# Kernel optimization log

Measured on AMD Instinct MI355X. Metric: run time of the kernel, lower is better.

The kernel has to match this reference:

```python
import jax, jax.numpy as jnp
import numpy as np


def _maxpool3d(x):
    # 3x3x3 max pool, stride 1, padding 1 (torch pads with -inf for max pool)
    return jax.lax.reduce_window(
        x, -jnp.inf, jax.lax.max,
        window_dimensions=(1, 1, 3, 3, 3),
        window_strides=(1, 1, 1, 1, 1),
        padding=[(0, 0), (0, 0), (1, 1), (1, 1), (1, 1)],
    )


def _soft_erode(x):
    return -_maxpool3d(-x)


def _soft_dilate(x):
    return _maxpool3d(x)


def _soft_open(x):
    return _soft_dilate(_soft_erode(x))


def setup_inputs() -> dict:
    key = jax.random.key(0)
    img = jax.random.uniform(key, (2, 1, 192, 256, 256), dtype=jnp.float32)
    return {"img": img}


def reference(img):
    # NOTE: in the original torch module, `skel` is computed via soft_close +
    # an iterative relu(skel - soft_open(skel)) loop, but the final line
    # `skel = F.relu(img - soft_open(img))` overwrites it entirely, so the
    # loop is dead code and the output depends only on img.
    opened = _soft_open(img)  # dilate(erode(img)), morphological opening
    return jax.nn.relu(img - opened)
```

## Files before the change

### kernel.cpp

```cpp
#include <hip/hip_runtime.h>
#include <math.h>


#define D_ 192
#define H_ 256
#define W_ 256
#define NB 2
#define TH 32
#define TW 64
#define CD 16
#define NCHUNK (D_ / CD)

#define RAW_H (TH + 4)
#define RAW_W (TW + 8)
#define RAW_S 76
#define EB_H  (TH + 2)
#define EB_W  (TW + 8)
#define EB_S  76

#define NRAWF4 (RAW_H * (RAW_W / 4))
#define NBTASK (EB_H * (EB_W / 8))

__device__ __forceinline__ float min3f(float a, float b, float c) {
    return fminf(fminf(a, b), c);
}
__device__ __forceinline__ float max3f(float a, float b, float c) {
    return fmaxf(fmaxf(a, b), c);
}

__global__ __launch_bounds__(256, 3)
void soft_skel_v2(const float* __restrict__ img, float* __restrict__ out) {
    __shared__ __align__(16) float raw[RAW_H][RAW_S];
    __shared__ __align__(16) float ebuf[EB_H][EB_S];

    const int tid = threadIdx.x;
    const int w0 = blockIdx.x * TW;
    const int h0 = blockIdx.y * TH;
    const int n  = blockIdx.z / NCHUNK;
    const int ch = blockIdx.z - n * NCHUNK;
    const int z0 = ch * CD;

    const float* vol  = img + (size_t)n * (D_ * H_ * W_);
    float*       ovol = out + (size_t)n * (D_ * H_ * W_);

    const float PINF = INFINITY;

    bool a_slot[3], a_img[3];
    int  a_lds[3], a_off[3];
    #pragma unroll
    for (int k = 0; k < 3; ++k) {
        int idx = tid + 256 * k;
        bool slot = idx < NRAWF4;
        int row = idx / (RAW_W / 4);
        int cg  = idx - row * (RAW_W / 4);
        int gh = h0 - 2 + row;
        int gw = w0 - 4 + 4 * cg;
        a_slot[k] = slot;
        a_img[k]  = slot && (gh >= 0) && (gh < H_) && (gw >= 0) && (gw <= W_ - 4);
        a_off[k]  = gh * W_ + gw;
        a_lds[k]  = slot ? (row * RAW_S + 4 * cg) : 0;
    }

    const int  r0 = tid / 9;
    const int  c0 = (tid - r0 * 9) * 8;
    const bool has1 = tid < (NBTASK - 256);
    const int  t1 = tid + 256;
    const int  r1 = t1 / 9;
    const int  c1 = (t1 - r1 * 9) * 8;

    const int ty = tid >> 3;
    const int xx = (tid & 7) * 8;

    float pm0[8], sp0[8], pm1[8], sp1[8];
    float t2A[8], t2B[8], t2C[8];
    float rwA[8], rwB[8], rwC[8];
    #pragma unroll
    for (int j = 0; j < 8; ++j) {
        pm0[j] = sp0[j] = pm1[j] = sp1[j] = PINF;
        t2A[j] = t2B[j] = 0.f;
        rwA[j] = rwB[j] = 0.f;
    }

    auto prefetch = [&](int zz, float4 L[3]) {
        const bool zok = (zz >= 0) && (zz < D_);
        const float* plane = vol + (size_t)zz * (H_ * W_);
        #pragma unroll
        for (int k = 0; k < 3; ++k) {
            float4 v = make_float4(PINF, PINF, PINF, PINF);
            if (zok && a_img[k]) v = *(const float4*)(plane + a_off[k]);
            L[k] = v;
        }
    };

    auto btask = [&](int r, int cb, float pm[8], float sp[8], bool zeok) {
        float vm[10];
        {
            const float* p0 = &raw[r][0];
            const float* p1 = &raw[r + 1][0];
            const float* p2 = &raw[r + 2][0];
            int cl = cb - 1; if (cl < 0) cl = 0;
            int cr = cb + 8; if (cr > RAW_W - 1) cr = RAW_W - 1;
            vm[0] = min3f(p0[cl], p1[cl], p2[cl]);
            vm[9] = min3f(p0[cr], p1[cr], p2[cr]);
            float4 q00 = *(const float4*)(p0 + cb);
            float4 q01 = *(const float4*)(p0 + cb + 4);
            float4 q10 = *(const float4*)(p1 + cb);
            float4 q11 = *(const float4*)(p1 + cb + 4);
            float4 q20 = *(const float4*)(p2 + cb);
            float4 q21 = *(const float4*)(p2 + cb + 4);
            vm[1] = min3f(q00.x, q10.x, q20.x);
            vm[2] = min3f(q00.y, q10.y, q20.y);
            vm[3] = min3f(q00.z, q10.z, q20.z);
            vm[4] = min3f(q00.w, q10.w, q20.w);
            vm[5] = min3f(q01.x, q11.x, q21.x);
            vm[6] = min3f(q01.y, q11.y, q21.y);
            vm[7] = min3f(q01.z, q11.z, q21.z);
            vm[8] = min3f(q01.w, q11.w, q21.w);
        }
        float s[8];
        #pragma unroll
        for (int j = 0; j < 8; ++j) s[j] = min3f(vm[j], vm[j + 1], vm[j + 2]);

        const bool rok = zeok && ((unsigned)(h0 - 1 + r) < (unsigned)H_);
        float e[8];
        #pragma unroll
        for (int j = 0; j < 8; ++j) {
            float ev = fminf(pm[j], s[j]);
            bool ok = rok && ((unsigned)(w0 - 4 + cb + j) < (unsigned)W_);
            e[j] = ok ? ev : -PINF;
            pm[j] = fminf(sp[j], s[j]);
            sp[j] = s[j];
        }
        *(float4*)&ebuf[r][cb]     = make_float4(e[0], e[1], e[2], e[3]);
        *(float4*)&ebuf[r][cb + 4] = make_float4(e[4], e[5], e[6], e[7]);
    };

    float4 L[3];
    prefetch(z0 - 2, L);
    const int zzend = z0 + CD + 1;

    for (int zz = z0 - 2; zz <= zzend; ++zz) {
        #pragma unroll
        for (int k = 0; k < 3; ++k)
            if (a_slot[k]) *(float4*)(&raw[0][0] + a_lds[k]) = L[k];
        if (zz < zzend) prefetch(zz + 1, L);
        __syncthreads();

        {
            float4 v0 = *(const float4*)&raw[ty + 2][xx + 4];
            float4 v1 = *(const float4*)&raw[ty + 2][xx + 8];
            rwC[0] = v0.x; rwC[1] = v0.y; rwC[2] = v0.z; rwC[3] = v0.w;
            rwC[4] = v1.x; rwC[5] = v1.y; rwC[6] = v1.z; rwC[7] = v1.w;
        }

        const int  ze   = zz - 1;
        const bool zeok = (ze >= 0) && (ze < D_);
        btask(r0, c0, pm0, sp0, zeok);
        if (has1) btask(r1, c1, pm1, sp1, zeok);
        __syncthreads();

        {
            float vm[10];
            const float* p0 = &ebuf[ty][0];
            const float* p1 = &ebuf[ty + 1][0];
            const float* p2 = &ebuf[ty + 2][0];
            vm[0] = max3f(p0[xx + 3], p1[xx + 3], p2[xx + 3]);
            vm[9] = max3f(p0[xx + 12], p1[xx + 12], p2[xx + 12]);
            float4 q00 = *(const float4*)(p0 + xx + 4);
            float4 q01 = *(const float4*)(p0 + xx + 8);
            float4 q10 = *(const float4*)(p1 + xx + 4);
            float4 q11 = *(const float4*)(p1 + xx + 8);
            float4 q20 = *(const float4*)(p2 + xx + 4);
            float4 q21 = *(const float4*)(p2 + xx + 8);
            vm[1] = max3f(q00.x, q10.x, q20.x);
            vm[2] = max3f(q00.y, q10.y, q20.y);
            vm[3] = max3f(q00.z, q10.z, q20.z);
            vm[4] = max3f(q00.w, q10.w, q20.w);
            vm[5] = max3f(q01.x, q11.x, q21.x);
            vm[6] = max3f(q01.y, q11.y, q21.y);
            vm[7] = max3f(q01.z, q11.z, q21.z);
            vm[8] = max3f(q01.w, q11.w, q21.w);
            #pragma unroll
            for (int j = 0; j < 8; ++j) t2C[j] = max3f(vm[j], vm[j + 1], vm[j + 2]);
        }

        if (zz >= z0 + 2) {
            const int z = zz - 2;
            float* op = ovol + ((size_t)z * H_ + (h0 + ty)) * W_ + (w0 + xx);
            float o[8];
            #pragma unroll
            for (int j = 0; j < 8; ++j) {
                float opened = max3f(t2A[j], t2B[j], t2C[j]);
                float v = rwA[j] - opened;
                o[j] = v > 0.f ? v : 0.f;
            }
            *(float4*)op       = make_float4(o[0], o[1], o[2], o[3]);
            *(float4*)(op + 4) = make_float4(o[4], o[5], o[6], o[7]);
        }

        #pragma unroll
        for (int j = 0; j < 8; ++j) {
            t2A[j] = t2B[j]; t2B[j] = t2C[j];
            rwA[j] = rwB[j]; rwB[j] = rwC[j];
        }
    }
}

extern "C" void kernel_launch(void* const* d_in, const int* in_sizes, int n_in,
                              void* d_out, int out_size, void* d_ws, size_t ws_size,
                              hipStream_t stream) {
    const float* img = (const float*)d_in[0];
    float* out = (float*)d_out;

    dim3 grid(W_ / TW, H_ / TH, NB * NCHUNK);
    dim3 block(256);
    soft_skel_v2<<<grid, block, 0, stream>>>(img, out);
}
```

Before: 195.0 us.

## Compute two output rows per thread with triple-buffered swizzled LDS planes

Each thread now computes two adjacent rows in both the erode and dilate stages, so the overlapping vertical min/max across shared rows is computed once and reused. The raw plane buffer becomes three-deep, so the centre values are read from the buffered plane instead of being carried in registers. LDS rows are padded and swizzled to reduce bank conflicts. Only 128 threads now do the dilate/output stage, and launch bounds drop to 2 blocks per SM, which raises LDS and register use and may lower occupancy.

```diff
diff --git a/kernel.cpp b/kernel.cpp
--- a/kernel.cpp
+++ b/kernel.cpp
@@ -11,16 +11,14 @@
 #define CD 16
 #define NCHUNK (D_ / CD)
 
-#define RAW_H (TH + 4)
-#define RAW_W (TW + 8)
-#define RAW_S 76
-#define EB_H  (TH + 2)
-#define EB_W  (TW + 8)
-#define EB_S  76
-
-#define NRAWF4 (RAW_H * (RAW_W / 4))
-#define NBTASK (EB_H * (EB_W / 8))
-
+#define RS 88
+#define RAW_ROWS 36
+#define EB_ROWS 34
+#define RAW_SZ (RAW_ROWS * RS)
+#define EB_SZ  (EB_ROWS * RS)
+#define NRAWF4 (RAW_ROWS * 18)
+
+__device__ __forceinline__ int rbase(int r) { return r * RS + 4 * ((r >> 1) & 3); }
 __device__ __forceinline__ float min3f(float a, float b, float c) {
     return fminf(fminf(a, b), c);
 }
@@ -28,10 +26,10 @@
     return fmaxf(fmaxf(a, b), c);
 }
 
-__global__ __launch_bounds__(256, 3)
-void soft_skel_v2(const float* __restrict__ img, float* __restrict__ out) {
-    __shared__ __align__(16) float raw[RAW_H][RAW_S];
-    __shared__ __align__(16) float ebuf[EB_H][EB_S];
+__global__ __launch_bounds__(256, 2)
+void soft_skel_v10(const float* __restrict__ img, float* __restrict__ out) {
+    __shared__ __align__(16) float raw[3][RAW_SZ];
+    __shared__ __align__(16) float ebuf[EB_SZ];
 
     const int tid = threadIdx.x;
     const int w0 = blockIdx.x * TW;
@@ -42,7 +40,6 @@
 
     const float* vol  = img + (size_t)n * (D_ * H_ * W_);
     float*       ovol = out + (size_t)n * (D_ * H_ * W_);
-
     const float PINF = INFINITY;
 
     bool a_slot[3], a_img[3];
@@ -51,37 +48,47 @@
     for (int k = 0; k < 3; ++k) {
         int idx = tid + 256 * k;
         bool slot = idx < NRAWF4;
-        int row = idx / (RAW_W / 4);
-        int cg  = idx - row * (RAW_W / 4);
+        int row = idx / 18;
+        int cg  = idx - row * 18;
         int gh = h0 - 2 + row;
         int gw = w0 - 4 + 4 * cg;
         a_slot[k] = slot;
         a_img[k]  = slot && (gh >= 0) && (gh < H_) && (gw >= 0) && (gw <= W_ - 4);
         a_off[k]  = gh * W_ + gw;
-        a_lds[k]  = slot ? (row * RAW_S + 4 * cg) : 0;
+        a_lds[k]  = slot ? (rbase(row) + 4 * cg) : 0;
     }
 
-    const int  r0 = tid / 9;
-    const int  c0 = (tid - r0 * 9) * 8;
-    const bool has1 = tid < (NBTASK - 256);
-    const int  t1 = tid + 256;
-    const int  r1 = t1 / 9;
-    const int  c1 = (t1 - r1 * 9) * 8;
-
-    const int ty = tid >> 3;
-    const int xx = (tid & 7) * 8;
-
-    float pm0[8], sp0[8], pm1[8], sp1[8];
-    float t2A[8], t2B[8], t2C[8];
-    float rwA[8], rwB[8], rwC[8];
+    const int  bt   = (tid & 63) * 4 + (tid >> 6);
+    const bool bact = bt < 17 * 9;
+    const int  brg  = bt / 9;
+    const int  bcb  = (bt - brg * 9) * 8;
+    int rB[4];
+    #pragma unroll
+    for (int i = 0; i < 4; ++i) rB[i] = rbase(2 * brg + i);
+    const int bcolL = (bcb - 1 < 0) ? 0 : bcb - 1;
+    const int bcolR = (bcb + 8 > 71) ? 71 : bcb + 8;
+
+    const bool dact = tid < 128;
+    const int  drg  = tid >> 3;
+    const int  dxx  = (tid & 7) * 8;
+    int rD[4];
+    #pragma unroll
+    for (int i = 0; i < 4; ++i) rD[i] = rbase(2 * drg + i);
+
+    float pmA[8], spA[8], pmB[8], spB[8];
+    float tA1[8], tA2[8], tB1[8], tB2[8];
+    float t2CA[8], t2CB[8];
+    float cvA[8], cvB[8];
     #pragma unroll
     for (int j = 0; j < 8; ++j) {
-        pm0[j] = sp0[j] = pm1[j] = sp1[j] = PINF;
-        t2A[j] = t2B[j] = 0.f;
-        rwA[j] = rwB[j] = 0.f;
+        pmA[j] = spA[j] = pmB[j] = spB[j] = PINF;
+        tA1[j] = tA2[j] = tB1[j] = tB2[j] = 0.f;
+        t2CA[j] = t2CB[j] = 0.f;
+        cvA[j] = cvB[j] = 0.f;
     }
 
-    auto prefetch = [&](int zz, float4 L[3]) {
+    float4 L[3];
+    auto prefetch = [&](int zz) {
         const bool zok = (zz >= 0) && (zz < D_);
         const float* plane = vol + (size_t)zz * (H_ * W_);
         #pragma unroll
@@ -92,117 +99,150 @@
         }
     };
 
-    auto btask = [&](int r, int cb, float pm[8], float sp[8], bool zeok) {
-        float vm[10];
-        {
-            const float* p0 = &raw[r][0];
-            const float* p1 = &raw[r + 1][0];
-            const float* p2 = &raw[r + 2][0];
-            int cl = cb - 1; if (cl < 0) cl = 0;
-            int cr = cb + 8; if (cr > RAW_W - 1) cr = RAW_W - 1;
-            vm[0] = min3f(p0[cl], p1[cl], p2[cl]);
-            vm[9] = min3f(p0[cr], p1[cr], p2[cr]);
-            float4 q00 = *(const float4*)(p0 + cb);
-            float4 q01 = *(const float4*)(p0 + cb + 4);
-            float4 q10 = *(const float4*)(p1 + cb);
-            float4 q11 = *(const float4*)(p1 + cb + 4);
-            float4 q20 = *(const float4*)(p2 + cb);
-            float4 q21 = *(const float4*)(p2 + cb + 4);
-            vm[1] = min3f(q00.x, q10.x, q20.x);
-            vm[2] = min3f(q00.y, q10.y, q20.y);
-            vm[3] = min3f(q00.z, q10.z, q20.z);
-            vm[4] = min3f(q00.w, q10.w, q20.w);
-            vm[5] = min3f(q01.x, q11.x, q21.x);
-            vm[6] = min3f(q01.y, q11.y, q21.y);
-            vm[7] = min3f(q01.z, q11.z, q21.z);
-            vm[8] = min3f(q01.w, q11.w, q21.w);
-        }
-        float s[8];
-        #pragma unroll
-        for (int j = 0; j < 8; ++j) s[j] = min3f(vm[j], vm[j + 1], vm[j + 2]);
-
-        const bool rok = zeok && ((unsigned)(h0 - 1 + r) < (unsigned)H_);
-        float e[8];
-        #pragma unroll
-        for (int j = 0; j < 8; ++j) {
-            float ev = fminf(pm[j], s[j]);
-            bool ok = rok && ((unsigned)(w0 - 4 + cb + j) < (unsigned)W_);
-            e[j] = ok ? ev : -PINF;
-            pm[j] = fminf(sp[j], s[j]);
-            sp[j] = s[j];
-        }
-        *(float4*)&ebuf[r][cb]     = make_float4(e[0], e[1], e[2], e[3]);
-        *(float4*)&ebuf[r][cb + 4] = make_float4(e[4], e[5], e[6], e[7]);
-    };
-
-    float4 L[3];
-    prefetch(z0 - 2, L);
+    prefetch(z0 - 2);
+    int cur = 0;
     const int zzend = z0 + CD + 1;
 
     for (int zz = z0 - 2; zz <= zzend; ++zz) {
+        const int snxt = (cur == 2) ? 0 : cur + 1;
+
         #pragma unroll
         for (int k = 0; k < 3; ++k)
-            if (a_slot[k]) *(float4*)(&raw[0][0] + a_lds[k]) = L[k];
-        if (zz < zzend) prefetch(zz + 1, L);
+            if (a_slot[k]) *(float4*)&raw[cur][a_lds[k]] = L[k];
+        if (zz < zzend) prefetch(zz + 1);
         __syncthreads();
 
-        {
-            float4 v0 = *(const float4*)&raw[ty + 2][xx + 4];
-            float4 v1 = *(const float4*)&raw[ty + 2][xx + 8];
-            rwC[0] = v0.x; rwC[1] = v0.y; rwC[2] = v0.z; rwC[3] = v0.w;
-            rwC[4] = v1.x; rwC[5] = v1.y; rwC[6] = v1.z; rwC[7] = v1.w;
-        }
-
-        const int  ze   = zz - 1;
-        const bool zeok = (ze >= 0) && (ze < D_);
-        btask(r0, c0, pm0, sp0, zeok);
-        if (has1) btask(r1, c1, pm1, sp1, zeok);
+        const bool zeok = (unsigned)(zz - 1) < (unsigned)D_;
+        if (bact) {
+            const float* rp = raw[cur];
+            float q[4][8];
+            #pragma unroll
+            for (int i = 0; i < 4; ++i) {
+                float4 a = *(const float4*)&rp[rB[i] + bcb];
+                float4 b = *(const float4*)&rp[rB[i] + bcb + 4];
+                q[i][0] = a.x; q[i][1] = a.y; q[i][2] = a.z; q[i][3] = a.w;
+                q[i][4] = b.x; q[i][5] = b.y; q[i][6] = b.z; q[i][7] = b.w;
+            }
+            float vA[8], vB[8];
+            #pragma unroll
+            for (int j = 0; j < 8; ++j) {
+                float m = fminf(q[1][j], q[2][j]);
+                vA[j] = fminf(q[0][j], m);
+                vB[j] = fminf(m, q[3][j]);
+            }
+            float sLc[4], sRc[4];
+            #pragma unroll
+            for (int i = 0; i < 4; ++i) {
+                sLc[i] = rp[rB[i] + bcolL];
+                sRc[i] = rp[rB[i] + bcolR];
+            }
+            float mL = fminf(sLc[1], sLc[2]), mR = fminf(sRc[1], sRc[2]);
+            float vLA = fminf(sLc[0], mL), vLB = fminf(mL, sLc[3]);
+            float vRA = fminf(sRc[0], mR), vRB = fminf(mR, sRc[3]);
+
+            float sA[8], sB[8];
+            sA[0] = min3f(vLA, vA[0], vA[1]);
+            sB[0] = min3f(vLB, vB[0], vB[1]);
+            #pragma unroll
+            for (int j = 1; j < 7; ++j) {
+                sA[j] = min3f(vA[j - 1], vA[j], vA[j + 1]);
+                sB[j] = min3f(vB[j - 1], vB[j], vB[j + 1]);
+            }
+            sA[7] = min3f(vA[6], vA[7], vRA);
+            sB[7] = min3f(vB[6], vB[7], vRB);
+
+            const bool rokA = zeok && ((unsigned)(h0 - 1 + 2 * brg) < (unsigned)H_);
+            const bool rokB = zeok && ((unsigned)(h0 + 2 * brg) < (unsigned)H_);
+            float eA[8], eB[8];
+            #pragma unroll
+            for (int j = 0; j < 8; ++j) {
+                bool okc = (unsigned)(w0 - 4 + bcb + j) < (unsigned)W_;
+                eA[j] = (rokA && okc) ? fminf(pmA[j], sA[j]) : -PINF;
+                eB[j] = (rokB && okc) ? fminf(pmB[j], sB[j]) : -PINF;
+                pmA[j] = fminf(spA[j], sA[j]); spA[j] = sA[j];
+                pmB[j] = fminf(spB[j], sB[j]); spB[j] = sB[j];
+            }
+            *(float4*)&ebuf[rB[0] + bcb]     = make_float4(eA[0], eA[1], eA[2], eA[3]);
+            *(float4*)&ebuf[rB[0] + bcb + 4] = make_float4(eA[4], eA[5], eA[6], eA[7]);
+            *(float4*)&ebuf[rB[1] + bcb]     = make_float4(eB[0], eB[1], eB[2], eB[3]);
+            *(float4*)&ebuf[rB[1] + bcb + 4] = make_float4(eB[4], eB[5], eB[6], eB[7]);
+        }
+
+        if (dact && zz >= z0 + 2) {
+            const float* cp = raw[snxt];
+            float4 a0 = *(const float4*)&cp[rD[2] + dxx + 4];
+            float4 a1 = *(const float4*)&cp[rD[2] + dxx + 8];
+            float4 b0 = *(const float4*)&cp[rD[3] + dxx + 4];
+            float4 b1 = *(const float4*)&cp[rD[3] + dxx + 8];
+            cvA[0] = a0.x; cvA[1] = a0.y; cvA[2] = a0.z; cvA[3] = a0.w;
+            cvA[4] = a1.x; cvA[5] = a1.y; cvA[6] = a1.z; cvA[7] = a1.w;
+            cvB[0] = b0.x; cvB[1] = b0.y; cvB[2] = b0.z; cvB[3] = b0.w;
+            cvB[4] = b1.x; cvB[5] = b1.y; cvB[6] = b1.z; cvB[7] = b1.w;
+        }
         __syncthreads();
 
-        {
-            float vm[10];
-            const float* p0 = &ebuf[ty][0];
-            const float* p1 = &ebuf[ty + 1][0];
-            const float* p2 = &ebuf[ty + 2][0];
-            vm[0] = max3f(p0[xx + 3], p1[xx + 3], p2[xx + 3]);
-            vm[9] = max3f(p0[xx + 12], p1[xx + 12], p2[xx + 12]);
-            float4 q00 = *(const float4*)(p0 + xx + 4);
-            float4 q01 = *(const float4*)(p0 + xx + 8);
-            float4 q10 = *(const float4*)(p1 + xx + 4);
-            float4 q11 = *(const float4*)(p1 + xx + 8);
-            float4 q20 = *(const float4*)(p2 + xx + 4);
-            float4 q21 = *(const float4*)(p2 + xx + 8);
-            vm[1] = max3f(q00.x, q10.x, q20.x);
-            vm[2] = max3f(q00.y, q10.y, q20.y);
-            vm[3] = max3f(q00.z, q10.z, q20.z);
-            vm[4] = max3f(q00.w, q10.w, q20.w);
-            vm[5] = max3f(q01.x, q11.x, q21.x);
-            vm[6] = max3f(q01.y, q11.y, q21.y);
-            vm[7] = max3f(q01.z, q11.z, q21.z);
-            vm[8] = max3f(q01.w, q11.w, q21.w);
-            #pragma unroll
-            for (int j = 0; j < 8; ++j) t2C[j] = max3f(vm[j], vm[j + 1], vm[j + 2]);
-        }
-
-        if (zz >= z0 + 2) {
+        if (dact) {
+            float q[4][8];
+            #pragma unroll
+            for (int i = 0; i < 4; ++i) {
+                float4 a = *(const float4*)&ebuf[rD[i] + dxx + 4];
+                float4 b = *(const float4*)&ebuf[rD[i] + dxx + 8];
+                q[i][0] = a.x; q[i][1] = a.y; q[i][2] = a.z; q[i][3] = a.w;
+                q[i][4] = b.x; q[i][5] = b.y; q[i][6] = b.z; q[i][7] = b.w;
+            }
+            float tA[8], tB[8];
+            #pragma unroll
+            for (int j = 0; j < 8; ++j) {
+                float m = fmaxf(q[1][j], q[2][j]);
+                tA[j] = fmaxf(q[0][j], m);
+                tB[j] = fmaxf(m, q[3][j]);
+            }
+            float eLc[4], eRc[4];
+            #pragma unroll
+            for (int i = 0; i < 4; ++i) {
+                eLc[i] = ebuf[rD[i] + dxx + 3];
+                eRc[i] = ebuf[rD[i] + dxx + 12];
+            }
+            float mL = fmaxf(eLc[1], eLc[2]), mR = fmaxf(eRc[1], eRc[2]);
+            float tLA = fmaxf(eLc[0], mL), tLB = fmaxf(mL, eLc[3]);
+            float tRA = fmaxf(eRc[0], mR), tRB = fmaxf(mR, eRc[3]);
+
+            t2CA[0] = max3f(tLA, tA[0], tA[1]);
+            t2CB[0] = max3f(tLB, tB[0], tB[1]);
+            #pragma unroll
+            for (int j = 1; j < 7; ++j) {
+                t2CA[j] = max3f(tA[j - 1], tA[j], tA[j + 1]);
+                t2CB[j] = max3f(tB[j - 1], tB[j], tB[j + 1]);
+            }
+            t2CA[7] = max3f(tA[6], tA[7], tRA);
+            t2CB[7] = max3f(tB[6], tB[7], tRB);
+        }
+
+        if (dact && zz >= z0 + 2) {
             const int z = zz - 2;
-            float* op = ovol + ((size_t)z * H_ + (h0 + ty)) * W_ + (w0 + xx);
-            float o[8];
-            #pragma unroll
-            for (int j = 0; j < 8; ++j) {
-                float opened = max3f(t2A[j], t2B[j], t2C[j]);
-                float v = rwA[j] - opened;
-                o[j] = v > 0.f ? v : 0.f;
-            }
-            *(float4*)op       = make_float4(o[0], o[1], o[2], o[3]);
-            *(float4*)(op + 4) = make_float4(o[4], o[5], o[6], o[7]);
-        }
-
-        #pragma unroll
-        for (int j = 0; j < 8; ++j) {
-            t2A[j] = t2B[j]; t2B[j] = t2C[j];
-            rwA[j] = rwB[j]; rwB[j] = rwC[j];
-        }
+            float* op = ovol + ((size_t)z * H_ + (h0 + 2 * drg)) * W_ + (w0 + dxx);
+            float oA[8], oB[8];
+            #pragma unroll
+            for (int j = 0; j < 8; ++j) {
+                float vA = cvA[j] - max3f(tA1[j], tA2[j], t2CA[j]);
+                float vB = cvB[j] - max3f(tB1[j], tB2[j], t2CB[j]);
+                oA[j] = vA > 0.f ? vA : 0.f;
+                oB[j] = vB > 0.f ? vB : 0.f;
+            }
+            *(float4*)op            = make_float4(oA[0], oA[1], oA[2], oA[3]);
+            *(float4*)(op + 4)      = make_float4(oA[4], oA[5], oA[6], oA[7]);
+            *(float4*)(op + W_)     = make_float4(oB[0], oB[1], oB[2], oB[3]);
+            *(float4*)(op + W_ + 4) = make_float4(oB[4], oB[5], oB[6], oB[7]);
+        }
+
+        if (dact) {
+            #pragma unroll
+            for (int j = 0; j < 8; ++j) {
+                tA1[j] = tA2[j]; tA2[j] = t2CA[j];
+                tB1[j] = tB2[j]; tB2[j] = t2CB[j];
+            }
+        }
+        cur = snxt;
     }
 }
 
@@ -214,5 +254,5 @@
 
     dim3 grid(W_ / TW, H_ / TH, NB * NCHUNK);
     dim3 block(256);
-    soft_skel_v2<<<grid, block, 0, stream>>>(img, out);
-}
+    soft_skel_v10<<<grid, block, 0, stream>>>(img, out);
+}
```

Result: slower. 205.3 us (+5.3%).
